# Kernel tuning notes

Hardware: AMD Instinct MI355X
Metric: run time of the kernel (lower is better)

The kernel has to match this reference:

```python
import jax, jax.numpy as jnp
import numpy as np

B, S = 4, 1024
VD, TD, HD = 1024, 768, 2048
NH = 16
HDIM = HD // NH
SCALE = HDIM ** -0.5
THRESH = 2.0 / 3.0


def bitnet_linear(x, w, b):
    # BitNet b1.58 eval-mode: per-tensor abs-mean scale, clamp, ternarize, dense matmul
    scale = jnp.clip(jnp.mean(jnp.abs(w)), 1e-5, 1000.0)
    wn = jnp.clip(w / scale, -10.0, 10.0)
    q = jnp.where(wn > THRESH, 1.0, jnp.where(wn < -THRESH, -1.0, 0.0))
    return x @ (q * scale).T + b


def layernorm(x, g, b, eps=1e-5):
    mu = jnp.mean(x, axis=-1, keepdims=True)
    var = jnp.mean(jnp.square(x - mu), axis=-1, keepdims=True)
    return (x - mu) * jax.lax.rsqrt(var + eps) * g + b


def setup_inputs() -> dict:
    key = jax.random.key(0)
    ks = jax.random.split(key, 8)
    return {
        "vision_features": jax.random.normal(ks[0], (B, VD), jnp.float32),
        "text_features": jax.random.normal(ks[1], (B, S, TD), jnp.float32),
        "text_mask": jnp.ones((B, S), dtype=bool),
        "w_vision_proj": jax.random.normal(ks[2], (HD, VD), jnp.float32),
        "b_vision_proj": jnp.zeros((HD,), jnp.float32),
        "w_text_proj": jax.random.normal(ks[3], (HD, TD), jnp.float32),
        "b_text_proj": jnp.zeros((HD,), jnp.float32),
        "w_text_qkv": jax.random.normal(ks[4], (3 * HD, HD), jnp.float32),
        "b_text_qkv": jnp.zeros((3 * HD,), jnp.float32),
        "ln_text_g": jnp.ones((HD,), jnp.float32),
        "ln_text_b": jnp.zeros((HD,), jnp.float32),
        "w_out": jax.random.normal(ks[5], (HD, HD), jnp.float32),
        "b_out": jnp.zeros((HD,), jnp.float32),
        "ln_cross_g": jnp.ones((HD,), jnp.float32),
        "ln_cross_b": jnp.zeros((HD,), jnp.float32),
    }


def reference(vision_features, text_features, text_mask,
              w_vision_proj, b_vision_proj, w_text_proj, b_text_proj,
              w_text_qkv, b_text_qkv, ln_text_g, ln_text_b,
              w_out, b_out, ln_cross_g, ln_cross_b):
    # projections into shared hidden space (BitNet ternary linears)
    vp = bitnet_linear(vision_features, w_vision_proj, b_vision_proj)        # [B, HD]
    tp = bitnet_linear(text_features, w_text_proj, b_text_proj)              # [B, S, HD]

    # --- text self-attention (no rel-pos bias: the rel-pos branch raises and is swallowed) ---
    tn = layernorm(tp, ln_text_g, ln_text_b)
    qkv = bitnet_linear(tn, w_text_qkv, b_text_qkv)                          # [B, S, 3*HD]
    qkv = qkv.reshape(B, S, 3, NH, HDIM).transpose(2, 0, 3, 1, 4)            # [3, B, H, S, hd]
    tq, tk, tv = qkv[0], qkv[1], qkv[2]
    attn = jnp.einsum('bhqd,bhkd->bhqk', tq, tk) * SCALE                     # [B, H, S, S]
    attn = jnp.where(text_mask[:, None, None, :], attn, -1e9)
    attn = jax.nn.softmax(attn, axis=-1)
    text_self = jnp.einsum('bhqk,bhkd->bhqd', attn, tv)
    text_self = text_self.transpose(0, 2, 1, 3).reshape(B, S, HD)
    text_self = tp + text_self                                               # residual (dropout=id in eval)

    # --- image-to-text attention ---
    # original repeats the single vision query over seq then means the (identical)
    # outputs; mathematically equal to a single-query attention.
    vq = vp.reshape(B, NH, 1, HDIM)                                          # [B, H, 1, hd]
    tk2 = text_self.reshape(B, S, NH, HDIM).transpose(0, 2, 1, 3)            # [B, H, S, hd]
    i2t = jnp.einsum('bhqd,bhkd->bhqk', vq, tk2) * SCALE                     # [B, H, 1, S]
    i2t = jnp.where(text_mask[:, None, None, :], i2t, -1e9)
    i2t = jax.nn.softmax(i2t, axis=-1)
    i2t_out = jnp.einsum('bhqk,bhkd->bhqd', i2t, tk2).reshape(B, HD)         # [B, HD]

    # --- text-to-image attention (single kv "token" per head -> softmax over size-1 axis) ---
    tq2 = text_self.reshape(B, S, NH, HDIM).transpose(0, 2, 1, 3)            # [B, H, S, hd]
    vk = vp.reshape(B, NH, 1, HDIM)                                          # [B, H, 1, hd]
    t2i = jnp.einsum('bhqd,bhkd->bhqk', tq2, vk) * SCALE                     # [B, H, S, 1]
    t2i = jax.nn.softmax(t2i, axis=-1)                                       # all ones (size-1 axis)
    t2i_out = jnp.einsum('bhqk,bhkd->bhqd', t2i, vk)                         # [B, H, S, hd]
    t2i_out = t2i_out.transpose(0, 2, 1, 3).reshape(B, S, HD)

    # --- fusion: shared BitNet output projection + cross norm (inferred continuation) ---
    fused_vision = layernorm(vp + bitnet_linear(i2t_out, w_out, b_out), ln_cross_g, ln_cross_b)
    fused_text = layernorm(text_self + bitnet_linear(t2i_out, w_out, b_out), ln_cross_g, ln_cross_b)
    return fused_vision, fused_text
```

## Files before the change

### kernel.cpp

```cpp
#include <hip/hip_runtime.h>


typedef unsigned short u16;
typedef unsigned int   u32;
typedef __attribute__((ext_vector_type(4))) float f32x4;
typedef __attribute__((ext_vector_type(8))) short short8;
typedef _Float16 half8 __attribute__((ext_vector_type(8)));

__device__ __forceinline__ u16 f2h(float x) {
    _Float16 h = (_Float16)x;
    return __builtin_bit_cast(u16, h);
}
__device__ __forceinline__ f32x4 mfmah(short8 a, short8 b, f32x4 c) {
    return __builtin_amdgcn_mfma_f32_16x16x32_f16(
        __builtin_bit_cast(half8, a), __builtin_bit_cast(half8, b), c, 0, 0, 0);
}
__device__ __forceinline__ void gload16(const void* g, void* l) {
    __builtin_amdgcn_global_load_lds((const __attribute__((address_space(1))) u32*)g,
                                     (__attribute__((address_space(3))) u32*)l, 16, 0, 0);
}

__device__ __forceinline__ float blockReduceSum256(float v, float* red) {
#pragma unroll
    for (int o = 32; o; o >>= 1) v += __shfl_down(v, o);
    int lane = threadIdx.x & 63, w = threadIdx.x >> 6;
    __syncthreads();
    if (lane == 0) red[w] = v;
    __syncthreads();
    return red[0] + red[1] + red[2] + red[3];
}

__global__ __launch_bounds__(256) void k_absmean4(const float* __restrict__ w0, const float* __restrict__ w1,
                                                  const float* __restrict__ w2, const float* __restrict__ w3,
                                                  int n40, int n41, int n42, int n43,
                                                  double* __restrict__ part) {
    int slot = blockIdx.x >> 8, b = blockIdx.x & 255;
    const float* w = (slot == 0) ? w0 : (slot == 1) ? w1 : (slot == 2) ? w2 : w3;
    int n4 = (slot == 0) ? n40 : (slot == 1) ? n41 : (slot == 2) ? n42 : n43;
    const float4* w4 = (const float4*)w;
    double s = 0.0;
    for (int i = b * 256 + threadIdx.x; i < n4; i += 65536) {
        float4 v = w4[i];
        s += (double)fabsf(v.x) + (double)fabsf(v.y) + (double)fabsf(v.z) + (double)fabsf(v.w);
    }
#pragma unroll
    for (int o = 32; o; o >>= 1) s += __shfl_down(s, o);
    __shared__ double p4[4];
    int lane = threadIdx.x & 63, w_ = threadIdx.x >> 6;
    if (lane == 0) p4[w_] = s;
    __syncthreads();
    if (threadIdx.x == 0) part[slot * 256 + b] = p4[0] + p4[1] + p4[2] + p4[3];
}

__global__ void k_finalize(const double* __restrict__ part, float* __restrict__ scf) {
    int w = threadIdx.x >> 6, lane = threadIdx.x & 63;
    double s = 0.0;
    for (int j = lane; j < 256; j += 64) s += part[w * 256 + j];
#pragma unroll
    for (int o = 32; o; o >>= 1) s += __shfl_down(s, o);
    if (lane == 0) {
        const double ns[4] = {2097152.0, 1572864.0, 12582912.0, 4194304.0};
        float v = (float)(s / ns[w]);
        v = fminf(fmaxf(v, 1e-5f), 1000.0f);
        scf[w] = v;
    }
}

__global__ __launch_bounds__(256) void k_quant(const float* __restrict__ w, u32* __restrict__ qd,
                                               int n2, const float* __restrict__ scf, int slot) {
    float s = scf[slot];
    const float th = 2.0f / 3.0f;
    for (int i = blockIdx.x * blockDim.x + threadIdx.x; i < n2; i += gridDim.x * blockDim.x) {
        float2 v = ((const float2*)w)[i];
        float wn0 = v.x / s, wn1 = v.y / s;
        u32 q0 = (wn0 > th) ? 0x3C00u : ((wn0 < -th) ? 0xBC00u : 0u);
        u32 q1 = (wn1 > th) ? 0x3C00u : ((wn1 < -th) ? 0xBC00u : 0u);
        qd[i] = q0 | (q1 << 16);
    }
}

__global__ __launch_bounds__(256) void k_tofp16(const float* __restrict__ x, u32* __restrict__ xs, int n2) {
    for (int i = blockIdx.x * blockDim.x + threadIdx.x; i < n2; i += gridDim.x * blockDim.x) {
        float2 v = ((const float2*)x)[i];
        xs[i] = (u32)f2h(v.x) | (((u32)f2h(v.y)) << 16);
    }
}

__global__ __launch_bounds__(256) void k_gemm(const u16* __restrict__ A, const u16* __restrict__ Bw,
                                              int K, int N, int NB_N,
                                              const float* __restrict__ scf, int slot,
                                              const float* __restrict__ bias,
                                              float* Cf, u16* Cp, int epi) {
    __shared__ __align__(16) u16 ldsA[2][128 * 64];
    __shared__ __align__(16) u16 ldsB[2][128 * 64];
    int m0 = (blockIdx.x / NB_N) * 128;
    int n0 = (blockIdx.x % NB_N) * 128;
    int t = threadIdx.x, lane = t & 63, w = t >> 6;
    int wm = (w >> 1) * 64, wn = (w & 1) * 64;
    f32x4 acc[4][4];
#pragma unroll
    for (int i = 0; i < 4; i++)
#pragma unroll
        for (int j = 0; j < 4; j++) acc[i][j] = (f32x4)(0.0f);

    auto STAGE = [&](int buf, int k0) {
#pragma unroll
        for (int i = 0; i < 4; i++) {
            int c = i * 256 + t;
            int row = c & 127, kg = c >> 7;
            const u16* ga = A + (size_t)(m0 + row) * K + (k0 + kg * 8);
            const u16* gb = Bw + (size_t)(n0 + row) * K + (k0 + kg * 8);
            int db = (i * 256 + w * 64) * 8;
            gload16(ga, ldsA[buf] + db);
            gload16(gb, ldsB[buf] + db);
        }
    };
    auto COMPUTE = [&](int buf) {
#pragma unroll
        for (int kk = 0; kk < 64; kk += 32) {
            int kg4 = (kk >> 3) + (lane >> 4);
            short8 av[4], bv[4];
#pragma unroll
            for (int mi = 0; mi < 4; mi++)
                av[mi] = *(const short8*)(ldsA[buf] + (size_t)(kg4 * 128 + wm + mi * 16 + (lane & 15)) * 8);
#pragma unroll
            for (int ni = 0; ni < 4; ni++)
                bv[ni] = *(const short8*)(ldsB[buf] + (size_t)(kg4 * 128 + wn + ni * 16 + (lane & 15)) * 8);
#pragma unroll
            for (int mi = 0; mi < 4; mi++)
#pragma unroll
                for (int ni = 0; ni < 4; ni++)
                    acc[mi][ni] = mfmah(av[mi], bv[ni], acc[mi][ni]);
        }
    };

    STAGE(0, 0);
    __syncthreads();
    int cur = 0;
    for (int k0 = 64; k0 < K; k0 += 64) {
        STAGE(cur ^ 1, k0);
        COMPUTE(cur);
        __syncthreads();
        cur ^= 1;
    }
    COMPUTE(cur);

    float s = scf[slot];
#pragma unroll
    for (int ni = 0; ni < 4; ni++) {
        int col = n0 + wn + ni * 16 + (lane & 15);
        float bv = bias[col];
#pragma unroll
        for (int mi = 0; mi < 4; mi++) {
            int rb = m0 + wm + mi * 16 + ((lane >> 4) << 2);
#pragma unroll
            for (int j = 0; j < 4; j++) {
                float y = acc[mi][ni][j] * s + bv;
                if (epi == 0) {
                    Cf[(size_t)(rb + j) * N + col] = y;
                } else {
                    Cp[(size_t)(rb + j) * N + col] = f2h(y);
                }
            }
        }
    }
}

__global__ __launch_bounds__(256) void k_vp(const float* __restrict__ vf, const float* __restrict__ w,
                                            const float* __restrict__ bias, const float* __restrict__ scf,
                                            float* __restrict__ vp) {
    __shared__ float xl[4096];
    int t = threadIdx.x;
#pragma unroll
    for (int i = 0; i < 16; i++) xl[t + i * 256] = vf[t + i * 256];
    __syncthreads();
    int lane = t & 63;
    int n = blockIdx.x * 4 + (t >> 6);
    float s = scf[0];
    const float th = 2.0f / 3.0f;
    float a0 = 0, a1 = 0, a2 = 0, a3 = 0;
    const float* wr = w + (size_t)n * 1024;
    for (int k = lane; k < 1024; k += 64) {
        float wn = wr[k] / s;
        float q = (wn > th) ? 1.0f : ((wn < -th) ? -1.0f : 0.0f);
        a0 += xl[k] * q; a1 += xl[1024 + k] * q; a2 += xl[2048 + k] * q; a3 += xl[3072 + k] * q;
    }
#pragma unroll
    for (int o = 32; o; o >>= 1) {
        a0 += __shfl_down(a0, o); a1 += __shfl_down(a1, o);
        a2 += __shfl_down(a2, o); a3 += __shfl_down(a3, o);
    }
    if (lane == 0) {
        float bv = bias[n];
        vp[n] = a0 * s + bv; vp[2048 + n] = a1 * s + bv;
        vp[4096 + n] = a2 * s + bv; vp[6144 + n] = a3 * s + bv;
    }
}

__global__ __launch_bounds__(256) void k_ln1(const float* __restrict__ x, const float* __restrict__ g,
                                             const float* __restrict__ b, u16* __restrict__ tn) {
    __shared__ float red[4];
    int r = blockIdx.x, t = threadIdx.x;
    const float* xr = x + (size_t)r * 2048;
    float v[8]; float s = 0;
#pragma unroll
    for (int i = 0; i < 8; i++) { v[i] = xr[t + i * 256]; s += v[i]; }
    s = blockReduceSum256(s, red);
    float mu = s * (1.0f / 2048.0f);
    float s2 = 0;
#pragma unroll
    for (int i = 0; i < 8; i++) { float d = v[i] - mu; s2 += d * d; }
    s2 = blockReduceSum256(s2, red);
    float rstd = 1.0f / sqrtf(s2 * (1.0f / 2048.0f) + 1e-5f);
#pragma unroll
    for (int i = 0; i < 8; i++) {
        int c = t + i * 256;
        float y = (v[i] - mu) * rstd * g[c] + b[c];
        tn[(size_t)r * 2048 + c] = f2h(y);
    }
}

__global__ __launch_bounds__(256) void k_attn(const u16* __restrict__ qkv, float* ts) {
    __shared__ __align__(16) u16 kp[8192];
    __shared__ __align__(16) u16 vt[128 * 72];
    int t = threadIdx.x, lane = t & 63, w = t >> 6;
    int bh = blockIdx.x >> 4, qb = blockIdx.x & 15;
    int b = bh >> 4, h = bh & 15;
    int rowbase = b * 1024;
    int q0 = qb * 64 + w * 16;
    u16* pl = kp + (size_t)w * 16 * 72;

    short8 qh[4];
    {
        int r = rowbase + q0 + (lane & 15);
        const u16* qp = qkv + (size_t)r * 6144 + h * 128 + (lane >> 4) * 8;
#pragma unroll
        for (int c4 = 0; c4 < 4; c4++) qh[c4] = *(const short8*)(qp + c4 * 32);
    }
    float m[4], ld[4];
#pragma unroll
    for (int j = 0; j < 4; j++) { m[j] = -1e30f; ld[j] = 0.0f; }
    f32x4 po[8];
#pragma unroll
    for (int nt = 0; nt < 8; nt++) po[nt] = (f32x4)(0.0f);
    const float SC = 0.08838834764831845f;

    for (int kt = 0; kt < 16; kt++) {
        __syncthreads();
#pragma unroll
        for (int i = 0; i < 4; i++) {
            int c = i * 256 + t;
            int sl = c & 63, dg = c >> 6;
            const u16* gk = qkv + (size_t)(rowbase + kt * 64 + sl) * 6144 + (2048 + h * 128 + dg * 8);
            gload16(gk, kp + (size_t)(i * 256 + w * 64) * 8);
        }
#pragma unroll
        for (int i = 0; i < 4; i++) {
            int c = i * 256 + t;
            int sl = c & 63, dg = c >> 6;
            const u16* gv = qkv + (size_t)(rowbase + kt * 64 + sl) * 6144 + (4096 + h * 128 + dg * 8);
            short8 vv = *(const short8*)gv;
#pragma unroll
            for (int j = 0; j < 8; j++) vt[(size_t)(dg * 8 + j) * 72 + sl] = (u16)vv[j];
        }
        __syncthreads();

        f32x4 sacc[4];
#pragma unroll
        for (int nt = 0; nt < 4; nt++) sacc[nt] = (f32x4)(0.0f);
#pragma unroll
        for (int c4 = 0; c4 < 4; c4++) {
            int kg = c4 * 4 + (lane >> 4);
#pragma unroll
            for (int nt = 0; nt < 4; nt++) {
                short8 kf = *(const short8*)(kp + (size_t)(kg * 64 + nt * 16 + (lane & 15)) * 8);
                sacc[nt] = mfmah(qh[c4], kf, sacc[nt]);
            }
        }
        float fsc[4], rs[4];
#pragma unroll
        for (int j = 0; j < 4; j++) {
            float mx = fmaxf(fmaxf(sacc[0][j], sacc[1][j]), fmaxf(sacc[2][j], sacc[3][j]));
            mx = fmaxf(mx, __shfl_xor(mx, 1));
            mx = fmaxf(mx, __shfl_xor(mx, 2));
            mx = fmaxf(mx, __shfl_xor(mx, 4));
            mx = fmaxf(mx, __shfl_xor(mx, 8));
            float mn = fmaxf(m[j], mx * SC);
            fsc[j] = expf(m[j] - mn);
            m[j] = mn; rs[j] = 0.0f;
        }
        __syncthreads();
#pragma unroll
        for (int nt = 0; nt < 4; nt++) {
#pragma unroll
            for (int j = 0; j < 4; j++) {
                float p = expf(sacc[nt][j] * SC - m[j]);
                rs[j] += p;
                pl[(size_t)((lane >> 4) * 4 + j) * 72 + nt * 16 + (lane & 15)] = f2h(p);
            }
        }
#pragma unroll
        for (int j = 0; j < 4; j++) {
            float r = rs[j];
            r += __shfl_xor(r, 1); r += __shfl_xor(r, 2);
            r += __shfl_xor(r, 4); r += __shfl_xor(r, 8);
            ld[j] = ld[j] * fsc[j] + r;
        }
#pragma unroll
        for (int nt = 0; nt < 8; nt++)
#pragma unroll
            for (int j = 0; j < 4; j++) po[nt][j] *= fsc[j];

#pragma unroll
        for (int kk2 = 0; kk2 < 2; kk2++) {
            short8 pa = *(const short8*)(pl + (size_t)(lane & 15) * 72 + kk2 * 32 + (lane >> 4) * 8);
#pragma unroll
            for (int nt = 0; nt < 8; nt++) {
                short8 vf = *(const short8*)(vt + (size_t)(nt * 16 + (lane & 15)) * 72 + kk2 * 32 + (lane >> 4) * 8);
                po[nt] = mfmah(pa, vf, po[nt]);
            }
        }
    }
#pragma unroll
    for (int nt = 0; nt < 8; nt++) {
        int d = nt * 16 + (lane & 15);
#pragma unroll
        for (int j = 0; j < 4; j++) {
            int r = rowbase + q0 + (lane >> 4) * 4 + j;
            size_t idx = (size_t)r * 2048 + h * 128 + d;
            ts[idx] = ts[idx] + po[nt][j] / ld[j];
        }
    }
}

__global__ __launch_bounds__(256) void k_i2t(const float* __restrict__ vp, const float* __restrict__ ts,
                                             float* __restrict__ io) {
    __shared__ float vq[128];
    __shared__ float sc[1024];
    __shared__ float red[4];
    __shared__ float part[256];
    int bh = blockIdx.x; int b = bh >> 4, h = bh & 15;
    int t = threadIdx.x, lane = t & 63, w = t >> 6;
    if (t < 128) vq[t] = vp[b * 2048 + h * 128 + t];
    __syncthreads();
    const float SC = 0.08838834764831845f;
    for (int s = w; s < 1024; s += 4) {
        const float* row = ts + (size_t)(b * 1024 + s) * 2048 + h * 128;
        float d = vq[lane] * row[lane] + vq[lane + 64] * row[lane + 64];
#pragma unroll
        for (int o = 32; o; o >>= 1) d += __shfl_down(d, o);
        if (lane == 0) sc[s] = d * SC;
    }
    __syncthreads();
    float mx = -1e30f;
    for (int s = t; s < 1024; s += 256) mx = fmaxf(mx, sc[s]);
#pragma unroll
    for (int o = 32; o; o >>= 1) mx = fmaxf(mx, __shfl_down(mx, o));
    if (lane == 0) red[w] = mx;
    __syncthreads();
    mx = fmaxf(fmaxf(red[0], red[1]), fmaxf(red[2], red[3]));
    __syncthreads();
    float sm = 0;
    for (int s = t; s < 1024; s += 256) { float p = expf(sc[s] - mx); sc[s] = p; sm += p; }
#pragma unroll
    for (int o = 32; o; o >>= 1) sm += __shfl_down(sm, o);
    if (lane == 0) red[w] = sm;
    __syncthreads();
    sm = red[0] + red[1] + red[2] + red[3];
    {
        int d = t & 127, sh = t >> 7;
        float acc = 0;
        const float* base = ts + (size_t)(b * 1024) * 2048 + h * 128 + d;
        for (int s = sh * 512; s < (sh + 1) * 512; s++) acc += sc[s] * base[(size_t)s * 2048];
        part[t] = acc;
    }
    __syncthreads();
    if (t < 128) io[b * 2048 + h * 128 + t] = (part[t] + part[128 + t]) / sm;
}

__global__ __launch_bounds__(256) void k_wout8(const float* __restrict__ i2t, const float* __restrict__ vp,
                                               const float* __restrict__ w, const float* __restrict__ bias,
                                               const float* __restrict__ scf, float* __restrict__ y8) {
    __shared__ float xl[8 * 2048];
    int t = threadIdx.x;
    for (int i = t; i < 16384; i += 256) {
        int rr = i >> 11, cc = i & 2047;
        xl[i] = (rr < 4) ? i2t[rr * 2048 + cc] : vp[(rr - 4) * 2048 + cc];
    }
    __syncthreads();
    int lane = t & 63;
    int n = blockIdx.x * 4 + (t >> 6);
    float s = scf[3];
    const float th = 2.0f / 3.0f;
    float a[8];
#pragma unroll
    for (int i = 0; i < 8; i++) a[i] = 0.0f;
    const float* wr = w + (size_t)n * 2048;
    for (int k = lane; k < 2048; k += 64) {
        float wn = wr[k] / s;
        float q = (wn > th) ? 1.0f : ((wn < -th) ? -1.0f : 0.0f);
#pragma unroll
        for (int i = 0; i < 8; i++) a[i] += xl[i * 2048 + k] * q;
    }
#pragma unroll
    for (int i = 0; i < 8; i++) {
#pragma unroll
        for (int o = 32; o; o >>= 1) a[i] += __shfl_down(a[i], o);
    }
    if (lane == 0) {
        float bv = bias[n];
#pragma unroll
        for (int i = 0; i < 8; i++) y8[i * 2048 + n] = a[i] * s + bv;
    }
}

__global__ __launch_bounds__(256) void k_fln(const float* __restrict__ xa, const float* __restrict__ y8,
                                             const float* __restrict__ g, const float* __restrict__ bb,
                                             float* __restrict__ out, int textmode) {
    __shared__ float red[4];
    int r = blockIdx.x, t = threadIdx.x;
    const float* a = xa + (size_t)r * 2048;
    const float* c = y8 + (size_t)(textmode ? (4 + (r >> 10)) : r) * 2048;
    float v[8]; float s = 0;
#pragma unroll
    for (int i = 0; i < 8; i++) { int cc = t + i * 256; v[i] = a[cc] + c[cc]; s += v[i]; }
    s = blockReduceSum256(s, red);
    float mu = s * (1.0f / 2048.0f);
    float s2 = 0;
#pragma unroll
    for (int i = 0; i < 8; i++) { float d = v[i] - mu; s2 += d * d; }
    s2 = blockReduceSum256(s2, red);
    float rstd = 1.0f / sqrtf(s2 * (1.0f / 2048.0f) + 1e-5f);
#pragma unroll
    for (int i = 0; i < 8; i++) {
        int cc = t + i * 256;
        out[(size_t)r * 2048 + cc] = (v[i] - mu) * rstd * g[cc] + bb[cc];
    }
}

extern "C" void kernel_launch(void* const* d_in, const int* in_sizes, int n_in,
                              void* d_out, int out_size, void* d_ws, size_t ws_size,
                              hipStream_t stream) {
    const float* vf    = (const float*)d_in[0];
    const float* tf    = (const float*)d_in[1];
    const float* w_vp  = (const float*)d_in[3];
    const float* b_vp  = (const float*)d_in[4];
    const float* w_tp  = (const float*)d_in[5];
    const float* b_tp  = (const float*)d_in[6];
    const float* w_qkv = (const float*)d_in[7];
    const float* b_qkv = (const float*)d_in[8];
    const float* lng   = (const float*)d_in[9];
    const float* lnb   = (const float*)d_in[10];
    const float* w_o   = (const float*)d_in[11];
    const float* b_o   = (const float*)d_in[12];
    const float* lcg   = (const float*)d_in[13];
    const float* lcb   = (const float*)d_in[14];
    float* out = (float*)d_out;
    char* ws = (char*)d_ws;

    constexpr size_t OFF_PART  = 0;
    constexpr size_t OFF_SCF   = 49152;
    constexpr size_t OFF_QDTP  = 65536;
    constexpr size_t OFF_QDQKV = 3276800;
    constexpr size_t OFF_XS    = 28442624;
    constexpr size_t OFF_TP    = 34734080;
    constexpr size_t OFF_TN    = 68288512;
    constexpr size_t OFF_QKV   = 85065728;
    constexpr size_t OFF_VP    = 135397376;
    constexpr size_t OFF_I2T   = 135430144;
    constexpr size_t OFF_Y8    = 135462912;

    double* part  = (double*)(ws + OFF_PART);
    float*  scf   = (float*)(ws + OFF_SCF);
    u16*   qd_tp  = (u16*)(ws + OFF_QDTP);
    u16*   qd_qkv = (u16*)(ws + OFF_QDQKV);
    u16*   xs     = (u16*)(ws + OFF_XS);
    float* tpb    = (float*)(ws + OFF_TP);
    u16*   tn     = (u16*)(ws + OFF_TN);
    u16*   qkvp   = (u16*)(ws + OFF_QKV);
    float* vpb    = (float*)(ws + OFF_VP);
    float* i2t    = (float*)(ws + OFF_I2T);
    float* y8     = (float*)(ws + OFF_Y8);

    k_absmean4<<<1024, 256, 0, stream>>>(w_vp, w_tp, w_qkv, w_o,
                                         2048 * 1024 / 4, 2048 * 768 / 4,
                                         6144 * 2048 / 4, 2048 * 2048 / 4, part);
    k_finalize<<<1, 256, 0, stream>>>(part, scf);

    k_quant<<<2048, 256, 0, stream>>>(w_tp,  (u32*)qd_tp,  2048 * 768  / 2, scf, 1);
    k_quant<<<4096, 256, 0, stream>>>(w_qkv, (u32*)qd_qkv, 6144 * 2048 / 2, scf, 2);
    k_tofp16<<<2048, 256, 0, stream>>>(tf, (u32*)xs, 4096 * 768 / 2);

    k_gemm<<<512, 256, 0, stream>>>(xs, qd_tp, 768, 2048, 16, scf, 1, b_tp, tpb, nullptr, 0);
    k_vp<<<512, 256, 0, stream>>>(vf, w_vp, b_vp, scf, vpb);

    k_ln1<<<4096, 256, 0, stream>>>(tpb, lng, lnb, tn);

    k_gemm<<<1536, 256, 0, stream>>>(tn, qd_qkv, 2048, 6144, 48, scf, 2, b_qkv, nullptr, qkvp, 1);

    k_attn<<<1024, 256, 0, stream>>>(qkvp, tpb);

    k_i2t<<<64, 256, 0, stream>>>(vpb, tpb, i2t);

    k_wout8<<<512, 256, 0, stream>>>(i2t, vpb, w_o, b_o, scf, y8);

    k_fln<<<4, 256, 0, stream>>>(vpb, y8, lcg, lcb, out, 0);
    k_fln<<<4096, 256, 0, stream>>>(tpb, y8, lcg, lcb, out + 8192, 1);
    (void)in_sizes; (void)n_in; (void)out_size; (void)ws_size;
}
```

Measured before the change: 677.3 us.

## Restructure GEMM to 128x256 tiles with 4-stage LDS pipeline and 512 threads

The GEMM kernel now uses 512-thread blocks computing 128x256 output tiles, with a 4-slot LDS ring buffer of 32-wide K slices. Loads run three stages ahead, gated by explicit vmcnt waits and a single barrier per iteration. The MFMA block is bracketed with s_setprio to favour the math waves. The goal is to hide global-load latency and cut barrier overhead, at the cost of more LDS per block and hand-tuned wait counts that depend on the exact number of loads per stage.

```diff
diff --git a/kernel.cpp b/kernel.cpp
--- a/kernel.cpp
+++ b/kernel.cpp
@@ -86,64 +86,70 @@
     }
 }
 
-__global__ __launch_bounds__(256) void k_gemm(const u16* __restrict__ A, const u16* __restrict__ Bw,
-                                              int K, int N, int NB_N,
-                                              const float* __restrict__ scf, int slot,
-                                              const float* __restrict__ bias,
-                                              float* Cf, u16* Cp, int epi) {
-    __shared__ __align__(16) u16 ldsA[2][128 * 64];
-    __shared__ __align__(16) u16 ldsB[2][128 * 64];
+__global__ __launch_bounds__(512, 2) void k_gemm(const u16* __restrict__ A, const u16* __restrict__ Bw,
+                                                 int K, int N, int NB_N,
+                                                 const float* __restrict__ scf, int slot,
+                                                 const float* __restrict__ bias,
+                                                 float* Cf, u16* Cp, int epi) {
+    __shared__ __align__(16) u16 sA[4][4096];
+    __shared__ __align__(16) u16 sB[4][8192];
+    int t = threadIdx.x, lane = t & 63, w = t >> 6;
     int m0 = (blockIdx.x / NB_N) * 128;
-    int n0 = (blockIdx.x % NB_N) * 128;
-    int t = threadIdx.x, lane = t & 63, w = t >> 6;
-    int wm = (w >> 1) * 64, wn = (w & 1) * 64;
+    int n0 = (blockIdx.x % NB_N) * 256;
+    int wm = (w >> 2) * 64, wn = (w & 3) * 64;
     f32x4 acc[4][4];
 #pragma unroll
     for (int i = 0; i < 4; i++)
 #pragma unroll
         for (int j = 0; j < 4; j++) acc[i][j] = (f32x4)(0.0f);
 
-    auto STAGE = [&](int buf, int k0) {
-#pragma unroll
-        for (int i = 0; i < 4; i++) {
-            int c = i * 256 + t;
-            int row = c & 127, kg = c >> 7;
-            const u16* ga = A + (size_t)(m0 + row) * K + (k0 + kg * 8);
-            const u16* gb = Bw + (size_t)(n0 + row) * K + (k0 + kg * 8);
-            int db = (i * 256 + w * 64) * 8;
-            gload16(ga, ldsA[buf] + db);
-            gload16(gb, ldsB[buf] + db);
+    const int NT = K >> 5;
+
+    auto STAGE = [&](int sl, int kt) {
+        int k0 = kt * 32;
+        {
+            int row = t & 127, kg = t >> 7;
+            gload16(A + (size_t)(m0 + row) * K + (k0 + kg * 8),
+                    sA[sl] + (size_t)(w * 64) * 8);
+        }
+#pragma unroll
+        for (int i = 0; i < 2; i++) {
+            int c = i * 512 + t;
+            int col = c & 255, kg = c >> 8;
+            gload16(Bw + (size_t)(n0 + col) * K + (k0 + kg * 8),
+                    sB[sl] + (size_t)(i * 512 + w * 64) * 8);
         }
     };
-    auto COMPUTE = [&](int buf) {
-#pragma unroll
-        for (int kk = 0; kk < 64; kk += 32) {
-            int kg4 = (kk >> 3) + (lane >> 4);
-            short8 av[4], bv[4];
-#pragma unroll
-            for (int mi = 0; mi < 4; mi++)
-                av[mi] = *(const short8*)(ldsA[buf] + (size_t)(kg4 * 128 + wm + mi * 16 + (lane & 15)) * 8);
+    auto COMPUTE = [&](int sl) {
+        short8 av[4], bv[4];
+#pragma unroll
+        for (int mi = 0; mi < 4; mi++)
+            av[mi] = *(const short8*)(sA[sl] + (size_t)((lane >> 4) * 128 + wm + mi * 16 + (lane & 15)) * 8);
+#pragma unroll
+        for (int ni = 0; ni < 4; ni++)
+            bv[ni] = *(const short8*)(sB[sl] + (size_t)((lane >> 4) * 256 + wn + ni * 16 + (lane & 15)) * 8);
+        __builtin_amdgcn_s_setprio(1);
+#pragma unroll
+        for (int mi = 0; mi < 4; mi++)
 #pragma unroll
             for (int ni = 0; ni < 4; ni++)
-                bv[ni] = *(const short8*)(ldsB[buf] + (size_t)(kg4 * 128 + wn + ni * 16 + (lane & 15)) * 8);
-#pragma unroll
-            for (int mi = 0; mi < 4; mi++)
-#pragma unroll
-                for (int ni = 0; ni < 4; ni++)
-                    acc[mi][ni] = mfmah(av[mi], bv[ni], acc[mi][ni]);
-        }
+                acc[mi][ni] = mfmah(av[mi], bv[ni], acc[mi][ni]);
+        __builtin_amdgcn_s_setprio(0);
     };
 
-    STAGE(0, 0);
-    __syncthreads();
-    int cur = 0;
-    for (int k0 = 64; k0 < K; k0 += 64) {
-        STAGE(cur ^ 1, k0);
-        COMPUTE(cur);
-        __syncthreads();
-        cur ^= 1;
-    }
-    COMPUTE(cur);
+    STAGE(0, 0); STAGE(1, 1); STAGE(2, 2);
+    for (int kt = 0; kt < NT - 2; ++kt) {
+        asm volatile("s_waitcnt vmcnt(6)" ::: "memory");
+        __builtin_amdgcn_s_barrier();
+        if (kt + 3 < NT) STAGE((kt + 3) & 3, kt + 3);
+        COMPUTE(kt & 3);
+    }
+    asm volatile("s_waitcnt vmcnt(3)" ::: "memory");
+    __builtin_amdgcn_s_barrier();
+    COMPUTE((NT - 2) & 3);
+    asm volatile("s_waitcnt vmcnt(0)" ::: "memory");
+    __builtin_amdgcn_s_barrier();
+    COMPUTE((NT - 1) & 3);
 
     float s = scf[slot];
 #pragma unroll
@@ -491,12 +497,12 @@
     k_quant<<<4096, 256, 0, stream>>>(w_qkv, (u32*)qd_qkv, 6144 * 2048 / 2, scf, 2);
     k_tofp16<<<2048, 256, 0, stream>>>(tf, (u32*)xs, 4096 * 768 / 2);
 
-    k_gemm<<<512, 256, 0, stream>>>(xs, qd_tp, 768, 2048, 16, scf, 1, b_tp, tpb, nullptr, 0);
+    k_gemm<<<256, 512, 0, stream>>>(xs, qd_tp, 768, 2048, 8, scf, 1, b_tp, tpb, nullptr, 0);
     k_vp<<<512, 256, 0, stream>>>(vf, w_vp, b_vp, scf, vpb);
 
     k_ln1<<<4096, 256, 0, stream>>>(tpb, lng, lnb, tn);
 
-    k_gemm<<<1536, 256, 0, stream>>>(tn, qd_qkv, 2048, 6144, 48, scf, 2, b_qkv, nullptr, qkvp, 1);
+    k_gemm<<<768, 512, 0, stream>>>(tn, qd_qkv, 2048, 6144, 24, scf, 2, b_qkv, nullptr, qkvp, 1);
 
     k_attn<<<1024, 256, 0, stream>>>(qkvp, tpb);
 
```

Result: slower. 697.7 us (+3.0%).

## Make QKV GEMM persistent over multiple tiles with cross-tile prefetch

Applied to the files above, without the earlier changes.

The GEMM kernel now lets each block process several consecutive output tiles. It streams the K-steps of all of them through one double-buffered pipeline, so the first stage of the next tile is prefetched while the current tile finishes and runs its epilogue. The QKV projection now launches 512 blocks that each handle 3 tiles instead of 1536 single-tile blocks, which removes the wave tail and per-block pipeline startup. The cost is less parallelism per launch, an epilogue that sits inside the main loop, and the need to reset the accumulators after each tile.

```diff
diff --git a/kernel.cpp b/kernel.cpp
--- a/kernel.cpp
+++ b/kernel.cpp
@@ -87,33 +87,41 @@
 }
 
 __global__ __launch_bounds__(256) void k_gemm(const u16* __restrict__ A, const u16* __restrict__ Bw,
-                                              int K, int N, int NB_N,
+                                              int K, int N, int NB_N, int TPB,
                                               const float* __restrict__ scf, int slot,
                                               const float* __restrict__ bias,
                                               float* Cf, u16* Cp, int epi) {
     __shared__ __align__(16) u16 ldsA[2][128 * 64];
     __shared__ __align__(16) u16 ldsB[2][128 * 64];
-    int m0 = (blockIdx.x / NB_N) * 128;
-    int n0 = (blockIdx.x % NB_N) * 128;
     int t = threadIdx.x, lane = t & 63, w = t >> 6;
     int wm = (w >> 1) * 64, wn = (w & 1) * 64;
+    const int NSTEP = K >> 6;
+    const int TOT = TPB * NSTEP;
+    int tile0 = blockIdx.x * TPB;
+
+    int sm0 = (tile0 / NB_N) * 128, sn = tile0 % NB_N, sk = 0;
+    int cm0 = sm0, cn = sn;
+
+    float s = scf[slot];
     f32x4 acc[4][4];
 #pragma unroll
     for (int i = 0; i < 4; i++)
 #pragma unroll
         for (int j = 0; j < 4; j++) acc[i][j] = (f32x4)(0.0f);
 
-    auto STAGE = [&](int buf, int k0) {
+    auto STAGE = [&](int buf) {
+        int k0 = sk * 64, n0 = sn * 128;
 #pragma unroll
         for (int i = 0; i < 4; i++) {
             int c = i * 256 + t;
             int row = c & 127, kg = c >> 7;
-            const u16* ga = A + (size_t)(m0 + row) * K + (k0 + kg * 8);
+            const u16* ga = A + (size_t)(sm0 + row) * K + (k0 + kg * 8);
             const u16* gb = Bw + (size_t)(n0 + row) * K + (k0 + kg * 8);
             int db = (i * 256 + w * 64) * 8;
             gload16(ga, ldsA[buf] + db);
             gload16(gb, ldsB[buf] + db);
         }
+        if (++sk == NSTEP) { sk = 0; if (++sn == NB_N) { sn = 0; sm0 += 128; } }
     };
     auto COMPUTE = [&](int buf) {
 #pragma unroll
@@ -133,36 +141,39 @@
                     acc[mi][ni] = mfmah(av[mi], bv[ni], acc[mi][ni]);
         }
     };
-
-    STAGE(0, 0);
-    __syncthreads();
-    int cur = 0;
-    for (int k0 = 64; k0 < K; k0 += 64) {
-        STAGE(cur ^ 1, k0);
+    auto EPILOGUE = [&]() {
+        int n0 = cn * 128;
+#pragma unroll
+        for (int ni = 0; ni < 4; ni++) {
+            int col = n0 + wn + ni * 16 + (lane & 15);
+            float bv = bias[col];
+#pragma unroll
+            for (int mi = 0; mi < 4; mi++) {
+                int rb = cm0 + wm + mi * 16 + ((lane >> 4) << 2);
+#pragma unroll
+                for (int j = 0; j < 4; j++) {
+                    float y = acc[mi][ni][j] * s + bv;
+                    if (epi == 0) {
+                        Cf[(size_t)(rb + j) * N + col] = y;
+                    } else {
+                        Cp[(size_t)(rb + j) * N + col] = f2h(y);
+                    }
+                    acc[mi][ni][j] = 0.0f;
+                }
+            }
+        }
+        if (++cn == NB_N) { cn = 0; cm0 += 128; }
+    };
+
+    STAGE(0);
+    __syncthreads();
+    int cur = 0, kc = 0;
+    for (int st = 0; st < TOT; st++) {
+        if (st + 1 < TOT) STAGE(cur ^ 1);
         COMPUTE(cur);
+        if (++kc == NSTEP) { kc = 0; EPILOGUE(); }
         __syncthreads();
         cur ^= 1;
-    }
-    COMPUTE(cur);
-
-    float s = scf[slot];
-#pragma unroll
-    for (int ni = 0; ni < 4; ni++) {
-        int col = n0 + wn + ni * 16 + (lane & 15);
-        float bv = bias[col];
-#pragma unroll
-        for (int mi = 0; mi < 4; mi++) {
-            int rb = m0 + wm + mi * 16 + ((lane >> 4) << 2);
-#pragma unroll
-            for (int j = 0; j < 4; j++) {
-                float y = acc[mi][ni][j] * s + bv;
-                if (epi == 0) {
-                    Cf[(size_t)(rb + j) * N + col] = y;
-                } else {
-                    Cp[(size_t)(rb + j) * N + col] = f2h(y);
-                }
-            }
-        }
     }
 }
 
@@ -491,12 +502,12 @@
     k_quant<<<4096, 256, 0, stream>>>(w_qkv, (u32*)qd_qkv, 6144 * 2048 / 2, scf, 2);
     k_tofp16<<<2048, 256, 0, stream>>>(tf, (u32*)xs, 4096 * 768 / 2);
 
-    k_gemm<<<512, 256, 0, stream>>>(xs, qd_tp, 768, 2048, 16, scf, 1, b_tp, tpb, nullptr, 0);
+    k_gemm<<<512, 256, 0, stream>>>(xs, qd_tp, 768, 2048, 16, 1, scf, 1, b_tp, tpb, nullptr, 0);
     k_vp<<<512, 256, 0, stream>>>(vf, w_vp, b_vp, scf, vpb);
 
     k_ln1<<<4096, 256, 0, stream>>>(tpb, lng, lnb, tn);
 
-    k_gemm<<<1536, 256, 0, stream>>>(tn, qd_qkv, 2048, 6144, 48, scf, 2, b_qkv, nullptr, qkvp, 1);
+    k_gemm<<<512, 256, 0, stream>>>(tn, qd_qkv, 2048, 6144, 48, 3, scf, 2, b_qkv, nullptr, qkvp, 1);
 
     k_attn<<<1024, 256, 0, stream>>>(qkvp, tpb);
 
```

Result: slower. 691.9 us (+2.2%).
